# Performance work log

Hardware: AMD Instinct MI355X
Metric: run time of the kernel (lower is better)

## Reference

```python
import jax, jax.numpy as jnp
import numpy as np

H = 512
N = 512
BSZ = 8
L = 4096
DIRECTION = 2  # 0=forward, 1=backward, 2=bidirectional (split N in half)


def setup_inputs() -> dict:
    key = jax.random.key(0)
    k = jax.random.split(key, 6)
    u = jax.random.normal(k[0], (BSZ, L, H), jnp.float32)
    # variable lengths in [L//2, L]
    lengths = jax.random.randint(k[1], (BSZ,), L // 2, L + 1).astype(jnp.int32)
    # LRU init: r_min=0, r_max=1, max_phase=2*pi
    u1 = jax.random.uniform(k[2], (N,), jnp.float32)
    nu_log = jnp.log(-0.5 * jnp.log(u1))
    u2 = jax.random.uniform(k[3], (N,), jnp.float32)
    theta_log = jnp.log(2.0 * np.pi * u2)
    lam = jnp.exp(-jnp.exp(nu_log) + 1j * jnp.exp(theta_log))  # (N,) complex
    gamma = jnp.sqrt(1.0 - jnp.abs(lam) ** 2)[:, None]          # (N,1)
    B = jax.random.normal(k[4], (H, N, 2), jnp.float32) / np.float32(np.sqrt(2 * H)) * gamma
    C = jax.random.normal(k[5], (2, H, N), jnp.float32) / np.float32(np.sqrt(N))
    return {"u": u, "lengths": lengths, "nu_log": nu_log, "theta_log": theta_log, "B": B, "C": C}


def _lru_scan(lam, Bu, reverse):
    """Diagonal linear recurrence x_t = lam * x_{t-1} + Bu_t along axis 2 via associative scan.
    lam: (n,) complex; Bu: (B, n, L) complex."""
    a = jnp.broadcast_to(lam[None, :, None], Bu.shape)

    def op(e1, e2):
        a1, b1 = e1
        a2, b2 = e2
        return a1 * a2, a2 * b1 + b2

    _, x = jax.lax.associative_scan(op, (a, Bu), axis=2, reverse=reverse)
    return x


def reference(u, lengths, nu_log, theta_log, B, C):
    lam = jnp.exp(-jnp.exp(nu_log) + 1j * jnp.exp(theta_log))  # (N,)
    Bc = B[..., 0] + 1j * B[..., 1]                            # (H, N) complex
    Bu = jnp.einsum('blh,hn->bnl', u, Bc)                      # (B, N, L) complex
    mask = jnp.arange(L)[None, :] < lengths[:, None]           # (B, L)
    Bu = Bu * mask[:, None, :]
    if DIRECTION == 2:
        h = N // 2
        x = jnp.concatenate([
            _lru_scan(lam[:h], Bu[:, :h], reverse=False),
            _lru_scan(lam[h:], Bu[:, h:], reverse=True),
        ], axis=1)
    elif DIRECTION == 0:
        x = _lru_scan(lam, Bu, reverse=False)
    else:
        x = _lru_scan(lam, Bu, reverse=True)
    x = x * mask[:, None, :]           # zero outputs past each sequence length
    x = jnp.swapaxes(x, 1, 2)          # (B, L, N)
    y = x.real @ C[0] - x.imag @ C[1]  # (B, L, H)  (requires H == N, as in source)
    return y
```

## Files before the change

### kernel.cpp

```cpp
#include <hip/hip_runtime.h>

#define L_SEQ   4096
#define BSZQ    8
#define ROWS    (BSZQ * L_SEQ)
#define KC1     512
#define NC1     1024
#define KC2     1024
#define NC2     512
#define CHUNK   64
#define NCHUNK  64

typedef __attribute__((ext_vector_type(8))) short bfrag;
typedef __attribute__((ext_vector_type(4))) float ffrag;

static __device__ __forceinline__ unsigned short f2bf(float f) {
    union { float f; unsigned int u; } v; v.f = f;
    unsigned int r = v.u + 0x7fffu + ((v.u >> 16) & 1u);
    return (unsigned short)(r >> 16);
}
static __device__ __forceinline__ unsigned int pk2(float a, float b) {
    return (unsigned int)f2bf(a) | ((unsigned int)f2bf(b) << 16);
}
static __device__ __forceinline__ float2 unpk2(unsigned int u) {
    union { unsigned int u; float f; } a, b;
    a.u = u << 16;
    b.u = u & 0xffff0000u;
    return make_float2(a.f, b.f);
}

static __device__ __forceinline__ void async16(const void* g, void* l) {
    __builtin_amdgcn_global_load_lds(
        (const __attribute__((address_space(1))) unsigned int*)g,
        (__attribute__((address_space(3))) unsigned int*)l,
        16, 0, 0);
}

__global__ __launch_bounds__(512) void lru_lam_kernel(
    const float* __restrict__ nu_log, const float* __restrict__ theta_log,
    float2* __restrict__ lam)
{
    int n = threadIdx.x;
    float mag = expf(-expf(nu_log[n]));
    float th  = expf(theta_log[n]);
    lam[n] = make_float2(mag * cosf(th), mag * sinf(th));
}

__global__ __launch_bounds__(256) void conv_mask_kernel(
    const float* __restrict__ u, const int* __restrict__ lengths,
    unsigned short* __restrict__ ub)
{
    int idx = blockIdx.x * 256 + threadIdx.x;
    int row = idx >> 6;
    int l = row & (L_SEQ - 1), b = row >> 12;
    bool keep = (l < lengths[b]);
    union { unsigned int s[4]; float4 f; } o;
    if (keep) {
        const float4 a = *(const float4*)(u + (size_t)idx * 8);
        const float4 c = *(const float4*)(u + (size_t)idx * 8 + 4);
        o.s[0] = pk2(a.x, a.y); o.s[1] = pk2(a.z, a.w);
        o.s[2] = pk2(c.x, c.y); o.s[3] = pk2(c.z, c.w);
    } else {
        o.s[0] = o.s[1] = o.s[2] = o.s[3] = 0u;
    }
    *(float4*)(ub + (size_t)idx * 8) = o.f;
}

__global__ __launch_bounds__(256) void prep_Bt_kernel(
    const float* __restrict__ B, unsigned short* __restrict__ Bt)
{
    int idx = blockIdx.x * 256 + threadIdx.x;
    int n2 = idx >> 9, h = idx & 511;
    Bt[idx] = f2bf(B[(size_t)h * 1024 + n2]);
}

__global__ __launch_bounds__(256) void prep_Dt_kernel(
    const float* __restrict__ C, unsigned short* __restrict__ Dt)
{
    int idx = blockIdx.x * 256 + threadIdx.x;
    int j = idx >> 10, k = idx & 1023;
    int n = k >> 1, c = k & 1;
    float v = C[((size_t)c * 512 + n) * 512 + j];
    Dt[idx] = f2bf(c ? -v : v);
}

template<int KD, int ND, bool BF16OUT>
__global__ __launch_bounds__(256) void mfma_gemm_async(
    const unsigned short* __restrict__ A,
    const unsigned short* __restrict__ Bt,
    void* __restrict__ Co)
{
    __shared__ __align__(16) char smem[32 * 132 * 4];
    uint4* As = (uint4*)smem;
    uint4* Bs = As + 512;
    float* Ts = (float*)smem;

    const int tid  = threadIdx.x;
    const int row0 = blockIdx.x * 128;
    const int col0 = blockIdx.y * 128;
    const int lane = tid & 63, w = tid >> 6;
    const int q = lane >> 4, m16 = lane & 15;
    const int wr = (w >> 1) * 64, wc = (w & 1) * 64;

    ffrag acc[4][4];
#pragma unroll
    for (int i = 0; i < 4; i++)
#pragma unroll
        for (int j = 0; j < 4; j++) acc[i][j] = (ffrag)0.f;

    for (int kt = 0; kt < KD; kt += 32) {
#pragma unroll
        for (int i = 0; i < 2; i++) {
            int t = i * 256 + w * 64 + lane;
            int r = t >> 2, kq = t & 3;
            async16(A  + (size_t)(row0 + r) * KD + kt + kq * 8, &As[i * 256 + w * 64]);
            async16(Bt + (size_t)(col0 + r) * KD + kt + kq * 8, &Bs[i * 256 + w * 64]);
        }
        __syncthreads();

        bfrag a[4], b[4];
#pragma unroll
        for (int ri = 0; ri < 4; ri++)
            a[ri] = *(bfrag*)&As[(wr + ri * 16 + m16) * 4 + q];
#pragma unroll
        for (int ci = 0; ci < 4; ci++)
            b[ci] = *(bfrag*)&Bs[(wc + ci * 16 + m16) * 4 + q];
#pragma unroll
        for (int ri = 0; ri < 4; ri++)
#pragma unroll
            for (int ci = 0; ci < 4; ci++)
                acc[ri][ci] = __builtin_amdgcn_mfma_f32_16x16x32_bf16(
                    a[ri], b[ci], acc[ri][ci], 0, 0, 0);
        __syncthreads();
    }

    if (BF16OUT) {
        unsigned int* Cb = (unsigned int*)Co;
        const int colc0 = col0 >> 1;
#pragma unroll
        for (int g = 0; g < 4; g++) {
            if (g) __syncthreads();
            if (wr == (g >> 1) * 64) {
                int gw = g & 1;
#pragma unroll
                for (int rj = 0; rj < 2; rj++) {
                    int ri = gw * 2 + rj;
#pragma unroll
                    for (int r4 = 0; r4 < 4; r4++) {
                        int rsl = rj * 16 + q * 4 + r4;
#pragma unroll
                        for (int ci = 0; ci < 4; ci++)
                            Ts[rsl * 132 + wc + ci * 16 + m16] = acc[ri][ci][r4];
                    }
                }
            }
            __syncthreads();
#pragma unroll
            for (int i = 0; i < 8; i++) {
                int flat = i * 256 + tid;
                int r = flat >> 6, cu = flat & 63;
                float2 v = *(float2*)&Ts[r * 132 + cu * 2];
                Cb[(size_t)(row0 + g * 32 + r) * (ND / 2) + colc0 + cu] =
                    pk2(v.x, v.y);
            }
        }
    } else {
        float* Cf = (float*)Co;
#pragma unroll
        for (int ri = 0; ri < 4; ri++)
#pragma unroll
            for (int r4 = 0; r4 < 4; r4++) {
                int row = row0 + wr + ri * 16 + q * 4 + r4;
#pragma unroll
                for (int ci = 0; ci < 4; ci++) {
                    int col = col0 + wc + ci * 16 + m16;
                    Cf[(size_t)row * ND + col] = acc[ri][ci][r4];
                }
            }
    }
}

__global__ __launch_bounds__(512) void scan_states_kernel(
    const unsigned int* __restrict__ bu, const float2* __restrict__ lam,
    float2* __restrict__ states)
{
    int n = threadIdx.x;
    int b = blockIdx.x >> 6;
    int c = blockIdx.x & 63;
    float2 lm = lam[n];
    float xr = 0.f, xi = 0.f;
    bool fwd = (n < 256);
    int l0 = fwd ? (c * CHUNK) : (c * CHUNK + CHUNK - 1);
    const unsigned int* p = bu + ((size_t)b * L_SEQ + l0) * 512 + n;
    ptrdiff_t step = fwd ? 512 : -512;
#pragma unroll 8
    for (int t = 0; t < CHUNK; t++) {
        float2 v = unpk2(*p);
        float nr = lm.x * xr - lm.y * xi + v.x;
        float ni = lm.x * xi + lm.y * xr + v.y;
        xr = nr; xi = ni;
        p += step;
    }
    states[((size_t)b * NCHUNK + c) * 512 + n] = make_float2(xr, xi);
}

__global__ __launch_bounds__(512) void scan_combine_kernel(
    const float2* __restrict__ states, float2* __restrict__ carries,
    const float2* __restrict__ lam)
{
    int n = threadIdx.x;
    int b = blockIdx.x;
    float2 lm = lam[n];
    float ar = lm.x, ai = lm.y;
#pragma unroll
    for (int i = 0; i < 6; i++) {
        float nr = ar * ar - ai * ai;
        ai = 2.f * ar * ai;
        ar = nr;
    }
    float cr = 0.f, ci = 0.f;
    bool fwd = (n < 256);
    if (fwd) {
        for (int c = 0; c < NCHUNK; c++) {
            size_t idx = ((size_t)b * NCHUNK + c) * 512 + n;
            carries[idx] = make_float2(cr, ci);
            float2 s = states[idx];
            float nr = ar * cr - ai * ci + s.x;
            float ni = ar * ci + ai * cr + s.y;
            cr = nr; ci = ni;
        }
    } else {
        for (int c = NCHUNK - 1; c >= 0; c--) {
            size_t idx = ((size_t)b * NCHUNK + c) * 512 + n;
            carries[idx] = make_float2(cr, ci);
            float2 s = states[idx];
            float nr = ar * cr - ai * ci + s.x;
            float ni = ar * ci + ai * cr + s.y;
            cr = nr; ci = ni;
        }
    }
}

__global__ __launch_bounds__(512) void scan_apply_kernel(
    unsigned int* __restrict__ bu, const float2* __restrict__ carries,
    const float2* __restrict__ lam, const int* __restrict__ lengths)
{
    int n = threadIdx.x;
    int b = blockIdx.x >> 6;
    int c = blockIdx.x & 63;
    int len = lengths[b];
    float2 lm = lam[n];
    float2 cy = carries[((size_t)b * NCHUNK + c) * 512 + n];
    bool fwd = (n < 256);
    int l0 = fwd ? (c * CHUNK) : (c * CHUNK + CHUNK - 1);
    int dl = fwd ? 1 : -1;
    unsigned int* p = bu + ((size_t)b * L_SEQ + l0) * 512 + n;
    ptrdiff_t step = fwd ? 512 : -512;
    float xr = cy.x, xi = cy.y;
    int l = l0;
#pragma unroll 8
    for (int t = 0; t < CHUNK; t++) {
        float2 v = unpk2(*p);
        float nr = lm.x * xr - lm.y * xi + v.x;
        float ni = lm.x * xi + lm.y * xr + v.y;
        xr = nr; xi = ni;
        *p = (l >= len) ? 0u : pk2(xr, xi);
        p += step; l += dl;
    }
}

extern "C" void kernel_launch(void* const* d_in, const int* in_sizes, int n_in,
                              void* d_out, int out_size, void* d_ws, size_t ws_size,
                              hipStream_t stream)
{
    const float* u        = (const float*)d_in[0];
    const int*   lengths  = (const int*)  d_in[1];
    const float* nu_log   = (const float*)d_in[2];
    const float* theta_log= (const float*)d_in[3];
    const float* B        = (const float*)d_in[4];
    const float* C        = (const float*)d_in[5];
    float* y = (float*)d_out;

    char* wp = (char*)d_ws;
    float2* lam     = (float2*)wp;  wp += 4096;
    float2* states  = (float2*)wp;  wp += (size_t)BSZQ * NCHUNK * 512 * 8;
    float2* carries = (float2*)wp;  wp += (size_t)BSZQ * NCHUNK * 512 * 8;
    unsigned int* bu = (unsigned int*)wp; wp += (size_t)ROWS * 512 * 4;
    unsigned short* ub = (unsigned short*)wp; wp += (size_t)ROWS * 512 * 2;
    unsigned short* Bt = (unsigned short*)wp; wp += (size_t)NC1 * KC1 * 2;
    unsigned short* Dt = (unsigned short*)wp; wp += (size_t)NC2 * KC2 * 2;

    lru_lam_kernel<<<1, 512, 0, stream>>>(nu_log, theta_log, lam);
    conv_mask_kernel<<<8192, 256, 0, stream>>>(u, lengths, ub);
    prep_Bt_kernel<<<2048, 256, 0, stream>>>(B, Bt);
    prep_Dt_kernel<<<2048, 256, 0, stream>>>(C, Dt);

    {
        dim3 grid(ROWS / 128, NC1 / 128);
        mfma_gemm_async<KC1, NC1, true><<<grid, 256, 0, stream>>>(ub, Bt, bu);
    }

    scan_states_kernel<<<BSZQ * NCHUNK, 512, 0, stream>>>(bu, lam, states);
    scan_combine_kernel<<<BSZQ, 512, 0, stream>>>(states, carries, lam);
    scan_apply_kernel<<<BSZQ * NCHUNK, 512, 0, stream>>>(bu, carries, lam, lengths);

    {
        dim3 grid(ROWS / 128, NC2 / 128);
        mfma_gemm_async<KC2, NC2, false><<<grid, 256, 0, stream>>>(
            (const unsigned short*)bu, Dt, y);
    }
}
```

Baseline: 298.4 us.

## Double-buffer GEMM LDS tiles with swizzle, fuse prep kernels, batch scan loads

Both GEMMs now double-buffer their LDS tiles so the async loads for the next K slice overlap the MFMA work on the current one. The tiles use an XOR swizzle to cut LDS bank conflicts, and launch bounds now ask for four blocks per SM. The bf16 epilogue packs pairs with lane shuffles instead of staging through LDS. The three small prep kernels are merged into one launch, and the scan combine loop batches eight state loads ahead of its serial recurrence. The trade-off is twice the LDS per block and a tighter register budget from the occupancy hint.

```diff
diff --git a/kernel.cpp b/kernel.cpp
--- a/kernel.cpp
+++ b/kernel.cpp
@@ -35,14 +35,32 @@
         16, 0, 0);
 }
 
-__global__ __launch_bounds__(512) void lru_lam_kernel(
+__global__ __launch_bounds__(256) void prep_all_kernel(
+    const float* __restrict__ B, const float* __restrict__ C,
     const float* __restrict__ nu_log, const float* __restrict__ theta_log,
+    unsigned short* __restrict__ Bt, unsigned short* __restrict__ Dt,
     float2* __restrict__ lam)
 {
-    int n = threadIdx.x;
-    float mag = expf(-expf(nu_log[n]));
-    float th  = expf(theta_log[n]);
-    lam[n] = make_float2(mag * cosf(th), mag * sinf(th));
+    int g = blockIdx.x, tid = threadIdx.x;
+    if (g < 2048) {
+        int idx = g * 256 + tid;
+        int n2 = idx >> 9, h = idx & 511;
+        Bt[idx] = f2bf(B[(size_t)h * 1024 + n2]);
+    } else if (g < 4096) {
+        int idx = (g - 2048) * 256 + tid;
+        int j = idx >> 10, k = idx & 1023;
+        int n = k >> 1, c = k & 1;
+        float v = C[((size_t)c * 512 + n) * 512 + j];
+        Dt[idx] = f2bf(c ? -v : v);
+    } else {
+#pragma unroll
+        for (int r = 0; r < 2; r++) {
+            int n = tid + r * 256;
+            float mag = expf(-expf(nu_log[n]));
+            float th  = expf(theta_log[n]);
+            lam[n] = make_float2(mag * cosf(th), mag * sinf(th));
+        }
+    }
 }
 
 __global__ __launch_bounds__(256) void conv_mask_kernel(
@@ -65,41 +83,21 @@
     *(float4*)(ub + (size_t)idx * 8) = o.f;
 }
 
-__global__ __launch_bounds__(256) void prep_Bt_kernel(
-    const float* __restrict__ B, unsigned short* __restrict__ Bt)
-{
-    int idx = blockIdx.x * 256 + threadIdx.x;
-    int n2 = idx >> 9, h = idx & 511;
-    Bt[idx] = f2bf(B[(size_t)h * 1024 + n2]);
-}
-
-__global__ __launch_bounds__(256) void prep_Dt_kernel(
-    const float* __restrict__ C, unsigned short* __restrict__ Dt)
-{
-    int idx = blockIdx.x * 256 + threadIdx.x;
-    int j = idx >> 10, k = idx & 1023;
-    int n = k >> 1, c = k & 1;
-    float v = C[((size_t)c * 512 + n) * 512 + j];
-    Dt[idx] = f2bf(c ? -v : v);
-}
-
 template<int KD, int ND, bool BF16OUT>
-__global__ __launch_bounds__(256) void mfma_gemm_async(
+__global__ __launch_bounds__(256, 4) void gemm_db(
     const unsigned short* __restrict__ A,
     const unsigned short* __restrict__ Bt,
     void* __restrict__ Co)
 {
-    __shared__ __align__(16) char smem[32 * 132 * 4];
-    uint4* As = (uint4*)smem;
-    uint4* Bs = As + 512;
-    float* Ts = (float*)smem;
+    __shared__ __align__(16) unsigned short As[2][128 * 32];
+    __shared__ __align__(16) unsigned short Bs[2][128 * 32];
 
     const int tid  = threadIdx.x;
-    const int row0 = blockIdx.x * 128;
-    const int col0 = blockIdx.y * 128;
     const int lane = tid & 63, w = tid >> 6;
     const int q = lane >> 4, m16 = lane & 15;
     const int wr = (w >> 1) * 64, wc = (w & 1) * 64;
+    const int row0 = blockIdx.x * 128;
+    const int col0 = blockIdx.y * 128;
 
     ffrag acc[4][4];
 #pragma unroll
@@ -107,23 +105,38 @@
 #pragma unroll
         for (int j = 0; j < 4; j++) acc[i][j] = (ffrag)0.f;
 
+#define STAGE_T(GP, TB, KT, GR0) do {                                          \
+    _Pragma("unroll")                                                          \
+    for (int j_ = 0; j_ < 2; j_++) {                                           \
+        int s_ = j_ * 256 + tid;                                               \
+        int r_ = s_ >> 2;                                                      \
+        int cs_ = (s_ & 3) ^ ((r_ >> 1) & 3);                                  \
+        async16(GP + (size_t)((GR0) + r_) * KD + (KT) + cs_ * 8,               \
+                &TB[(size_t)(j_ * 256 + w * 64) * 8]);                         \
+    }                                                                          \
+} while (0)
+
+    STAGE_T(A,  As[0], 0, row0);
+    STAGE_T(Bt, Bs[0], 0, col0);
+    __syncthreads();
+
+    int c = 0;
     for (int kt = 0; kt < KD; kt += 32) {
-#pragma unroll
-        for (int i = 0; i < 2; i++) {
-            int t = i * 256 + w * 64 + lane;
-            int r = t >> 2, kq = t & 3;
-            async16(A  + (size_t)(row0 + r) * KD + kt + kq * 8, &As[i * 256 + w * 64]);
-            async16(Bt + (size_t)(col0 + r) * KD + kt + kq * 8, &Bs[i * 256 + w * 64]);
-        }
-        __syncthreads();
-
+        if (kt + 32 < KD) {
+            STAGE_T(A,  As[c ^ 1], kt + 32, row0);
+            STAGE_T(Bt, Bs[c ^ 1], kt + 32, col0);
+        }
         bfrag a[4], b[4];
 #pragma unroll
-        for (int ri = 0; ri < 4; ri++)
-            a[ri] = *(bfrag*)&As[(wr + ri * 16 + m16) * 4 + q];
-#pragma unroll
-        for (int ci = 0; ci < 4; ci++)
-            b[ci] = *(bfrag*)&Bs[(wc + ci * 16 + m16) * 4 + q];
+        for (int ri = 0; ri < 4; ri++) {
+            int r_ = wr + ri * 16 + m16;
+            a[ri] = *(const bfrag*)&As[c][r_ * 32 + (q ^ ((r_ >> 1) & 3)) * 8];
+        }
+#pragma unroll
+        for (int ci = 0; ci < 4; ci++) {
+            int r_ = wc + ci * 16 + m16;
+            b[ci] = *(const bfrag*)&Bs[c][r_ * 32 + (q ^ ((r_ >> 1) & 3)) * 8];
+        }
 #pragma unroll
         for (int ri = 0; ri < 4; ri++)
 #pragma unroll
@@ -131,38 +144,28 @@
                 acc[ri][ci] = __builtin_amdgcn_mfma_f32_16x16x32_bf16(
                     a[ri], b[ci], acc[ri][ci], 0, 0, 0);
         __syncthreads();
-    }
+        c ^= 1;
+    }
+#undef STAGE_T
 
     if (BF16OUT) {
         unsigned int* Cb = (unsigned int*)Co;
-        const int colc0 = col0 >> 1;
-#pragma unroll
-        for (int g = 0; g < 4; g++) {
-            if (g) __syncthreads();
-            if (wr == (g >> 1) * 64) {
-                int gw = g & 1;
-#pragma unroll
-                for (int rj = 0; rj < 2; rj++) {
-                    int ri = gw * 2 + rj;
-#pragma unroll
-                    for (int r4 = 0; r4 < 4; r4++) {
-                        int rsl = rj * 16 + q * 4 + r4;
-#pragma unroll
-                        for (int ci = 0; ci < 4; ci++)
-                            Ts[rsl * 132 + wc + ci * 16 + m16] = acc[ri][ci][r4];
-                    }
+        const int colc0 = (col0 >> 1) + (w & 1) * 32;
+#pragma unroll
+        for (int ri = 0; ri < 4; ri++)
+#pragma unroll
+            for (int cp = 0; cp < 2; cp++)
+#pragma unroll
+                for (int r4 = 0; r4 < 4; r4++) {
+                    float a0 = acc[ri][cp * 2][r4];
+                    float a1 = acc[ri][cp * 2 + 1][r4];
+                    float b0 = __shfl_xor(a0, 1);
+                    float b1 = __shfl_xor(a1, 1);
+                    unsigned int uo = (m16 & 1) ? pk2(b1, a1) : pk2(a0, b0);
+                    int row = row0 + wr + ri * 16 + q * 4 + r4;
+                    int ccol = (cp * 2 + (m16 & 1)) * 8 + (m16 >> 1);
+                    Cb[(size_t)row * (ND / 2) + colc0 + ccol] = uo;
                 }
-            }
-            __syncthreads();
-#pragma unroll
-            for (int i = 0; i < 8; i++) {
-                int flat = i * 256 + tid;
-                int r = flat >> 6, cu = flat & 63;
-                float2 v = *(float2*)&Ts[r * 132 + cu * 2];
-                Cb[(size_t)(row0 + g * 32 + r) * (ND / 2) + colc0 + cu] =
-                    pk2(v.x, v.y);
-            }
-        }
     } else {
         float* Cf = (float*)Co;
 #pragma unroll
@@ -219,22 +222,19 @@
     }
     float cr = 0.f, ci = 0.f;
     bool fwd = (n < 256);
-    if (fwd) {
-        for (int c = 0; c < NCHUNK; c++) {
-            size_t idx = ((size_t)b * NCHUNK + c) * 512 + n;
-            carries[idx] = make_float2(cr, ci);
-            float2 s = states[idx];
-            float nr = ar * cr - ai * ci + s.x;
-            float ni = ar * ci + ai * cr + s.y;
-            cr = nr; ci = ni;
-        }
-    } else {
-        for (int c = NCHUNK - 1; c >= 0; c--) {
-            size_t idx = ((size_t)b * NCHUNK + c) * 512 + n;
-            carries[idx] = make_float2(cr, ci);
-            float2 s = states[idx];
-            float nr = ar * cr - ai * ci + s.x;
-            float ni = ar * ci + ai * cr + s.y;
+    for (int g = 0; g < 8; g++) {
+        float2 s[8];
+#pragma unroll
+        for (int k = 0; k < 8; k++) {
+            int c = fwd ? (g * 8 + k) : (63 - (g * 8 + k));
+            s[k] = states[((size_t)b * NCHUNK + c) * 512 + n];
+        }
+#pragma unroll
+        for (int k = 0; k < 8; k++) {
+            int c = fwd ? (g * 8 + k) : (63 - (g * 8 + k));
+            carries[((size_t)b * NCHUNK + c) * 512 + n] = make_float2(cr, ci);
+            float nr = ar * cr - ai * ci + s[k].x;
+            float ni = ar * ci + ai * cr + s[k].y;
             cr = nr; ci = ni;
         }
     }
@@ -289,14 +289,12 @@
     unsigned short* Bt = (unsigned short*)wp; wp += (size_t)NC1 * KC1 * 2;
     unsigned short* Dt = (unsigned short*)wp; wp += (size_t)NC2 * KC2 * 2;
 
-    lru_lam_kernel<<<1, 512, 0, stream>>>(nu_log, theta_log, lam);
+    prep_all_kernel<<<4097, 256, 0, stream>>>(B, C, nu_log, theta_log, Bt, Dt, lam);
     conv_mask_kernel<<<8192, 256, 0, stream>>>(u, lengths, ub);
-    prep_Bt_kernel<<<2048, 256, 0, stream>>>(B, Bt);
-    prep_Dt_kernel<<<2048, 256, 0, stream>>>(C, Dt);
 
     {
         dim3 grid(ROWS / 128, NC1 / 128);
-        mfma_gemm_async<KC1, NC1, true><<<grid, 256, 0, stream>>>(ub, Bt, bu);
+        gemm_db<KC1, NC1, true><<<grid, 256, 0, stream>>>(ub, Bt, bu);
     }
 
     scan_states_kernel<<<BSZQ * NCHUNK, 512, 0, stream>>>(bu, lam, states);
@@ -305,7 +303,7 @@
 
     {
         dim3 grid(ROWS / 128, NC2 / 128);
-        mfma_gemm_async<KC2, NC2, false><<<grid, 256, 0, stream>>>(
+        gemm_db<KC2, NC2, false><<<grid, 256, 0, stream>>>(
             (const unsigned short*)bu, Dt, y);
     }
 }
```

Result: faster. 272.1 us (-8.8%).
